# Kernel optimization log

Measured on AMD Instinct MI355X. Metric: run time of the kernel, lower is better.

## Reference

```python
import jax, jax.numpy as jnp
import numpy as np

WZ, WH, WW = 2, 6, 12
N = WZ * WH * WW            # 144 tokens per window
DIM, HEADS = 384, 12
HD = DIM // HEADS           # 32
TOW = (8 // WZ) * (48 // WH)  # type_of_windows = 32
NW = 96 // WW               # longitude windows = 8
B_ = 1 * TOW * NW           # 256
TABLE = (2 * WW - 1) * WH * WH * WZ * WZ  # 3312


def _position_index():
    zi = np.arange(WZ); zj = -np.arange(WZ) * WZ
    hi = np.arange(WH); hj = -np.arange(WH) * WH
    w = np.arange(WW)
    c1 = np.stack(np.meshgrid(zi, hi, w, indexing='ij')).reshape(3, -1)
    c2 = np.stack(np.meshgrid(zj, hj, w, indexing='ij')).reshape(3, -1)
    coords = (c1[:, :, None] - c2[:, None, :]).transpose(1, 2, 0)  # (N, N, 3)
    coords[:, :, 2] += WW - 1
    coords[:, :, 1] *= 2 * WW - 1
    coords[:, :, 0] *= (2 * WW - 1) * WH * WH
    return coords.sum(-1).reshape(-1).astype(np.int32)  # (N*N,)


def setup_inputs() -> dict:
    key = jax.random.key(0)
    ks = jax.random.split(key, 7)
    x = jax.random.normal(ks[0], (B_, N, DIM), dtype=jnp.float32)
    mask = jax.random.normal(ks[1], (NW, N, N), dtype=jnp.float32)
    w_qkv = jax.random.normal(ks[2], (DIM, 3 * DIM), dtype=jnp.float32) * 0.02
    b_qkv = jax.random.normal(ks[3], (3 * DIM,), dtype=jnp.float32) * 0.02
    w_out = jax.random.normal(ks[4], (DIM, DIM), dtype=jnp.float32) * 0.02
    b_out = jax.random.normal(ks[5], (DIM,), dtype=jnp.float32) * 0.02
    bias_table = jax.random.normal(ks[6], (TABLE, TOW, HEADS), dtype=jnp.float32) * 0.02
    position_index = jnp.asarray(_position_index())
    return {"x": x, "mask": mask, "w_qkv": w_qkv, "b_qkv": b_qkv,
            "w_out": w_out, "b_out": b_out, "bias_table": bias_table,
            "position_index": position_index}


def reference(x, mask, w_qkv, b_qkv, w_out, b_out, bias_table, position_index):
    Bw, n, C = x.shape
    scale = HD ** -0.5
    qkv = (x @ w_qkv + b_qkv).reshape(Bw, n, 3, HEADS, HD)
    qkv = jnp.transpose(qkv, (2, 0, 3, 1, 4))  # (3, Bw, H, N, hd)
    q, k, v = qkv[0] * scale, qkv[1], qkv[2]
    attn = jnp.einsum('bhnd,bhmd->bhnm', q, k)  # (Bw, H, N, N)
    # Earth-specific bias: gather table rows by position index, tiled per window group
    r = Bw // TOW
    bias = bias_table[jnp.tile(position_index, r)]          # (r*N*N, TOW, H)
    bias = bias.reshape(n, n, -1, HEADS)                    # (N, N, Bw, H)
    bias = jnp.transpose(bias, (2, 3, 0, 1))                # (Bw, H, N, N)
    attn = attn + bias
    nW = mask.shape[0]
    attn = attn.reshape(Bw // nW, nW, HEADS, n, n) + mask[None, :, None]
    attn = jax.nn.softmax(attn.reshape(Bw, HEADS, n, n), axis=-1)
    out = jnp.einsum('bhnm,bhmd->bhnd', attn, v)            # (Bw, H, N, hd)
    out = jnp.transpose(out, (0, 2, 1, 3)).reshape(Bw, n, C)
    return out @ w_out + b_out
```

## Files before the change

kernel.cpp:

```cpp
#include <hip/hip_runtime.h>
#include <hip/hip_fp16.h>
#include <cstdint>
#include <cstddef>

#define NQQ  (144*144)
#define SCALE 0.17677669529663687f

#define AOH   0ull
#define X16H  0ull
#define QH    14155776ull
#define KH    28311552ull
#define VH    42467328ull
#define WTH   56623104ull
#define WOTH  57065472ull
#define MASKH 57212928ull
#define BIASH 57378816ull
#define WS_NEED_BYTES ((BIASH + 3072ull * 2592ull) * 2ull)

typedef _Float16 half8  __attribute__((ext_vector_type(8)));
typedef _Float16 half4v __attribute__((ext_vector_type(4)));
typedef float    f32x4  __attribute__((ext_vector_type(4)));

typedef __attribute__((address_space(1))) const unsigned int guint;
typedef __attribute__((address_space(3))) unsigned int luint;
#define GLD16(g, l) __builtin_amdgcn_global_load_lds((guint*)(g), (luint*)(l), 16, 0, 0)

#define WAITV4 asm volatile("s_waitcnt vmcnt(4)" ::: "memory")
#define WAITV0 asm volatile("s_waitcnt vmcnt(0)" ::: "memory")

__launch_bounds__(256)
__global__ void k_prep(const float* __restrict__ X, _Float16* __restrict__ X16,
                       const float* __restrict__ Wq, _Float16* __restrict__ WqT,
                       const float* __restrict__ Wo, _Float16* __restrict__ WoT,
                       const float* __restrict__ M, _Float16* __restrict__ M16,
                       const float* __restrict__ table, const int* __restrict__ pidx,
                       _Float16* __restrict__ biasOut) {
    __shared__ __align__(16) char psm[13888];
    const int bid = blockIdx.x;
    const int t   = threadIdx.x;
    if (bid < 13824) {
        size_t i = (size_t)bid * 256 + t;
        float4 f = *(const float4*)&X[i * 4];
        _Float16 h[4] = {(_Float16)f.x, (_Float16)f.y, (_Float16)f.z, (_Float16)f.w};
        *(ushort4*)&X16[i * 4] = *(ushort4*)h;
        return;
    }
    if (bid >= 14130) {
        _Float16 (*sTb)[18] = (_Float16(*)[18])psm;
        int* rowsL = (int*)(psm + 13824);
        const int j      = bid - 14130;
        const int s_tile = j / 162;
        const int chunk  = j - s_tile * 162;
        const int i0     = chunk * 16;
        if (t < 16) rowsL[t] = pidx[8 * (i0 + t) + s_tile];
        __syncthreads();
#pragma unroll
        for (int rr = 0; rr < 16; ++rr) {
            int row = rowsL[rr];
            sTb[t][rr] = (_Float16)table[(size_t)row * 384 + t];
            if (t < 128) sTb[t + 256][rr] = (_Float16)table[(size_t)row * 384 + t + 256];
        }
        __syncthreads();
        unsigned int* ob = (unsigned int*)biasOut;
#pragma unroll
        for (int v = t; v < 3072; v += 256) {
            int i1h = v >> 3, dw = v & 7;
            ob[(size_t)(s_tile * 384 + i1h) * 1296 + chunk * 8 + dw] =
                *(const unsigned int*)&sTb[i1h][dw * 2];
        }
        return;
    }
    if (bid >= 13968) {
        size_t i = (size_t)(bid - 13968) * 256 + t;
        float4 f = *(const float4*)&M[i * 4];
        _Float16 h[4] = {(_Float16)f.x, (_Float16)f.y, (_Float16)f.z, (_Float16)f.w};
        *(ushort4*)&M16[i * 4] = *(ushort4*)h;
        return;
    }
    _Float16 (*sT)[72] = (_Float16(*)[72])psm;
    const float* W; _Float16* WT; int K, Cn, cb, kb;
    if (bid < 13932) {
        int j = bid - 13824;
        W = Wq; WT = WqT; K = 384; Cn = 1152;
        cb = (j % 18) * 64; kb = (j / 18) * 64;
    } else {
        int j = bid - 13932;
        W = Wo; WT = WoT; K = 384; Cn = 384;
        cb = (j % 6) * 64; kb = (j / 6) * 64;
    }
#pragma unroll
    for (int i = 0; i < 16; ++i) {
        int id = t + 256 * i;
        int kl = id >> 6, cl = id & 63;
        sT[cl][kl] = (_Float16)W[(size_t)(kb + kl) * Cn + cb + cl];
    }
    __syncthreads();
#pragma unroll
    for (int i = 0; i < 16; ++i) {
        int id = t + 256 * i;
        int cl = id >> 6, kl = id & 63;
        WT[(size_t)(cb + cl) * K + kb + kl] = sT[cl][kl];
    }
}

#define STAGE3(dA, dB, kk) do {                                   \
    GLD16(gA + (kk),          (char*)(dA) + t * 16);              \
    GLD16(gA + (kk) + 24576,  (char*)(dA) + t * 16 + 4096);       \
    GLD16(gB + (kk),          (char*)(dB) + t * 16);              \
    GLD16(gB + (kk) + 24576,  (char*)(dB) + t * 16 + 4096);       \
} while (0)

#define CSTEP(pA, pB) do {                                        \
    half8 a[4], b[4];                                             \
    _Pragma("unroll")                                             \
    for (int i = 0; i < 4; ++i) a[i] = *(const half8*)((pA) + i * 1024); \
    _Pragma("unroll")                                             \
    for (int j = 0; j < 4; ++j) b[j] = *(const half8*)((pB) + j * 1024); \
    _Pragma("unroll")                                             \
    for (int i = 0; i < 4; ++i)                                   \
    _Pragma("unroll")                                             \
        for (int j = 0; j < 4; ++j)                               \
            acc[i][j] = __builtin_amdgcn_mfma_f32_16x16x32_f16(a[i], b[j], acc[i][j], 0, 0, 0); \
} while (0)

#define GEMM_PIPE() do {                                          \
    STAGE3(sA[0], sB[0], 0);                                      \
    STAGE3(sA[1], sB[1], 32);                                     \
    _Pragma("unroll")                                             \
    for (int s = 0; s < 12; ++s) {                                \
        if (s < 11) { WAITV4; } else { WAITV0; }                  \
        __builtin_amdgcn_s_barrier();                             \
        if (s < 10) STAGE3(sA[(s + 2) % 3], sB[(s + 2) % 3], 32 * (s + 2)); \
        const char* pA = (const char*)sA[s % 3] + aoff;           \
        const char* pB = (const char*)sB[s % 3] + boff;           \
        CSTEP(pA, pB);                                            \
    }                                                             \
} while (0)

__launch_bounds__(256)
__global__ void k_qkv_gemm_mfma(const _Float16* __restrict__ X16,
                                const _Float16* __restrict__ WT,
                                const float* __restrict__ bq,
                                _Float16* __restrict__ ws16) {
    __shared__ __align__(16) _Float16 sA[3][4096];
    __shared__ __align__(16) _Float16 sB[3][4096];
    const int t    = threadIdx.x;
    const int lane = t & 63;
    const int w    = t >> 6;
    const int quad = lane >> 4;
    const int l15  = lane & 15;
    const int bid = blockIdx.x;
    const int wg  = (bid & 7) * 324 + (bid >> 3);
    const int cy  = wg % 9, rx = wg / 9;
    const int r0  = rx * 128, c0 = cy * 128;
    const int wr  = (w >> 1) * 64, wc = (w & 1) * 64;

    const int srow = t >> 2;
    const int skch = (t & 3) ^ ((t >> 3) & 3);
    const _Float16* gA = &X16[(size_t)(r0 + srow) * 384 + skch * 8];
    const _Float16* gB = &WT [(size_t)(c0 + srow) * 384 + skch * 8];

    const int swz16 = (quad ^ ((l15 >> 1) & 3)) * 16;
    const int aoff  = (wr + l15) * 64 + swz16;
    const int boff  = (wc + l15) * 64 + swz16;

    f32x4 acc[4][4] = {};

    GEMM_PIPE();

#pragma unroll
    for (int j = 0; j < 4; ++j) {
        int c  = c0 + wc + 16 * j + l15;
        int p  = c / 384;
        int hh = (c >> 5) % 12;
        int d0 = c & 31;
        float bias = bq[c];
        float sc   = (p == 0) ? SCALE : 1.0f;
        size_t base = (p == 0) ? QH : ((p == 1) ? KH : VH);
#pragma unroll
        for (int i = 0; i < 4; ++i) {
#pragma unroll
            for (int reg = 0; reg < 4; ++reg) {
                int r  = r0 + wr + 16 * i + quad * 4 + reg;
                int bw = r / 144;
                int n  = r - bw * 144;
                ws16[base + (((size_t)bw * 12 + hh) * 144 + n) * 32 + d0] =
                    (_Float16)((acc[i][j][reg] + bias) * sc);
            }
        }
    }
}

__launch_bounds__(576)
__global__ void k_attn_fused_mfma(const _Float16* __restrict__ ws16,
                                  const _Float16* __restrict__ mask16,
                                  const float* __restrict__ table,
                                  const int* __restrict__ pidx,
                                  const _Float16* __restrict__ bias_pre,
                                  _Float16* __restrict__ AO) {
    __shared__ __align__(16) char smem[27616];
    _Float16 (*sK)[40]   = (_Float16(*)[40])(smem);
    _Float16 (*sVT)[168] = (_Float16(*)[168])(smem + 11520);
    _Float16* sBias      = (_Float16*)(smem + 22272);

    const int bh = blockIdx.x;
    const int b  = bh / 12;
    const int h  = bh - b * 12;
    const int t  = threadIdx.x;
    const int w    = t >> 6;
    const int lane = t & 63;
    const int quad = lane >> 4;
    const int l15  = lane & 15;

    const int s_tile = b >> 5;
    const int i1     = b & 31;

    const _Float16* qg = ws16 + QH + (size_t)bh * 4608;
    const _Float16* kg = ws16 + KH + (size_t)bh * 4608;
    const _Float16* vg = ws16 + VH + (size_t)bh * 4608;

    half8 aq = *(const half8*)&qg[(size_t)(16 * w + l15) * 32 + quad * 8];

    {
        int row = t >> 2, ko = (t & 3) * 8;
        *(uint4*)&sK[row][ko] = *(const uint4*)&kg[row * 32 + ko];
    }
    for (int i = t; i < 2304; i += 576) {
        unsigned int u = ((const unsigned int*)vg)[i];
        int m  = i >> 4, d0 = (i & 15) * 2;
        int mp = m ^ ((d0 >> 3) << 3);
        sVT[d0][mp]     = ((const _Float16*)&u)[0];
        sVT[d0 + 1][mp] = ((const _Float16*)&u)[1];
    }
    if (t < 512) {
        int d = t & 31, m = 144 + (t >> 5);
        sVT[d][m ^ ((d >> 3) << 3)] = (_Float16)0;
    }
    if (bias_pre) {
        const _Float16* bg = bias_pre + (size_t)bh * 2592;
        for (int i2 = t; i2 < 648; i2 += 576) {
            uint2 wv = *(const uint2*)&bg[i2 * 4];
            int r18 = i2 / 36;
            int col = i2 * 4 - r18 * 144;
            *(uint2*)&sBias[r18 * 148 + col] = wv;
        }
    } else {
        for (int i = t; i < 2592; i += 576) {
            int row = pidx[8 * i + s_tile];
            int r18 = i / 144;
            sBias[r18 * 148 + (i - r18 * 144)] =
                (_Float16)table[(size_t)row * 384 + i1 * 12 + h];
        }
    }
    __syncthreads();

    f32x4 tj[9] = {};
#pragma unroll
    for (int j = 0; j < 9; ++j) {
        half8 bk = *(const half8*)&sK[16 * j + l15][quad * 8];
        tj[j] = __builtin_amdgcn_mfma_f32_16x16x32_f16(bk, aq, tj[j], 0, 0, 0);
    }

    const int q    = 16 * w + l15;
    const int nb18 = q % 18;
    const _Float16* mrow = mask16 + (size_t)(b & 7) * NQQ + (size_t)q * 144 + 4 * quad;
    uint2 mz[9];
#pragma unroll
    for (int j = 0; j < 9; ++j) mz[j] = *(const uint2*)&mrow[16 * j];
#pragma unroll
    for (int j = 0; j < 9; ++j) {
        uint2 bz = *(const uint2*)&sBias[nb18 * 148 + 16 * j + 4 * quad];
        const _Float16* bb = (const _Float16*)&bz;
        const _Float16* mm = (const _Float16*)&mz[j];
#pragma unroll
        for (int reg = 0; reg < 4; ++reg)
            tj[j][reg] += (float)bb[reg] + (float)mm[reg];
    }
    float rmax = tj[0][0];
#pragma unroll
    for (int j = 0; j < 9; ++j)
#pragma unroll
        for (int reg = 0; reg < 4; ++reg) rmax = fmaxf(rmax, tj[j][reg]);
    rmax = fmaxf(rmax, __shfl_xor(rmax, 16));
    rmax = fmaxf(rmax, __shfl_xor(rmax, 32));
    float rsum = 0.0f;
#pragma unroll
    for (int j = 0; j < 9; ++j)
#pragma unroll
        for (int reg = 0; reg < 4; ++reg) {
            tj[j][reg] = __expf(tj[j][reg] - rmax);
            rsum += tj[j][reg];
        }
    rsum += __shfl_xor(rsum, 16);
    rsum += __shfl_xor(rsum, 32);
    const float inv = 1.0f / rsum;

    unsigned int pkA[10], pkB[10];
    pkA[9] = 0u; pkB[9] = 0u;
#pragma unroll
    for (int j = 0; j < 9; ++j) {
        auto a2 = __builtin_amdgcn_cvt_pkrtz(tj[j][0] * inv, tj[j][1] * inv);
        auto b2 = __builtin_amdgcn_cvt_pkrtz(tj[j][2] * inv, tj[j][3] * inv);
        pkA[j] = *(unsigned int*)&a2;
        pkB[j] = *(unsigned int*)&b2;
    }

    const int src_lo = 32 * (quad & 1) + l15;
    const int src_hi = src_lo + 16;
    const bool selhi = (quad >> 1) != 0;
    f32x4 o[2] = {};
#pragma unroll
    for (int kt = 0; kt < 5; ++kt) {
        const int j0 = 2 * kt, j1 = 2 * kt + 1;
        unsigned int a0l = __shfl((int)pkA[j0], src_lo);
        unsigned int a1l = __shfl((int)pkA[j1], src_lo);
        unsigned int b0l = __shfl((int)pkB[j0], src_lo);
        unsigned int b1l = __shfl((int)pkB[j1], src_lo);
        unsigned int a0h = __shfl((int)pkA[j0], src_hi);
        unsigned int a1h = __shfl((int)pkA[j1], src_hi);
        unsigned int b0h = __shfl((int)pkB[j0], src_hi);
        unsigned int b1h = __shfl((int)pkB[j1], src_hi);
        union { uint4 u4; half8 h8; } bp;
        bp.u4.x = selhi ? a1l : a0l;
        bp.u4.y = selhi ? b1l : b0l;
        bp.u4.z = selhi ? a1h : a0h;
        bp.u4.w = selhi ? b1h : b0h;
#pragma unroll
        for (int dt = 0; dt < 2; ++dt) {
            const int vrow = dt * 16 + l15;
            half8 av = *(const half8*)&sVT[vrow][(kt * 32 + quad * 8) ^ ((vrow >> 3) << 3)];
            o[dt] = __builtin_amdgcn_mfma_f32_16x16x32_f16(av, bp.h8, o[dt], 0, 0, 0);
        }
    }

#pragma unroll
    for (int dt = 0; dt < 2; ++dt) {
        int d = dt * 16 + quad * 4;
        half4v hv;
#pragma unroll
        for (int reg = 0; reg < 4; ++reg) hv[reg] = (_Float16)o[dt][reg];
        *(half4v*)&AO[((size_t)b * 144 + q) * 384 + h * 32 + d] = hv;
    }
}

__launch_bounds__(256)
__global__ void k_out_gemm_mfma(const _Float16* __restrict__ A16,
                                const _Float16* __restrict__ WoT,
                                const float* __restrict__ bo,
                                float* __restrict__ out) {
    __shared__ __align__(16) _Float16 sA[3][4096];
    __shared__ __align__(16) _Float16 sB[3][4096];
    const int t    = threadIdx.x;
    const int lane = t & 63;
    const int w    = t >> 6;
    const int quad = lane >> 4;
    const int l15  = lane & 15;
    const int bid = blockIdx.x;
    const int wg  = (bid & 7) * 108 + (bid >> 3);
    const int cy  = wg % 3, rx = wg / 3;
    const int r0  = rx * 128, c0 = cy * 128;
    const int wr  = (w >> 1) * 64, wc = (w & 1) * 64;

    const int srow = t >> 2;
    const int skch = (t & 3) ^ ((t >> 3) & 3);
    const _Float16* gA = &A16[(size_t)(r0 + srow) * 384 + skch * 8];
    const _Float16* gB = &WoT[(size_t)(c0 + srow) * 384 + skch * 8];

    const int swz16 = (quad ^ ((l15 >> 1) & 3)) * 16;
    const int aoff  = (wr + l15) * 64 + swz16;
    const int boff  = (wc + l15) * 64 + swz16;

    f32x4 acc[4][4] = {};

    GEMM_PIPE();

#pragma unroll
    for (int j = 0; j < 4; ++j) {
        int c = c0 + wc + 16 * j + l15;
        float bias = bo[c];
#pragma unroll
        for (int i = 0; i < 4; ++i) {
#pragma unroll
            for (int reg = 0; reg < 4; ++reg) {
                int r = r0 + wr + 16 * i + quad * 4 + reg;
                out[(size_t)r * 384 + c] = acc[i][j][reg] + bias;
            }
        }
    }
}

extern "C" void kernel_launch(void* const* d_in, const int* in_sizes, int n_in,
                              void* d_out, int out_size, void* d_ws, size_t ws_size,
                              hipStream_t stream) {
    const float* x      = (const float*)d_in[0];
    const float* mask   = (const float*)d_in[1];
    const float* w_qkv  = (const float*)d_in[2];
    const float* b_qkv  = (const float*)d_in[3];
    const float* w_out  = (const float*)d_in[4];
    const float* b_out  = (const float*)d_in[5];
    const float* table  = (const float*)d_in[6];
    const int*   pidx   = (const int*)d_in[7];
    float* out = (float*)d_out;
    _Float16* ws16 = (_Float16*)d_ws;

    const bool pre = ws_size >= (size_t)WS_NEED_BYTES;
    _Float16* bias16 = pre ? (ws16 + BIASH) : (_Float16*)nullptr;

    hipLaunchKernelGGL(k_prep,          dim3(pre ? 15426 : 14130), dim3(256), 0, stream,
                       x, ws16 + X16H, w_qkv, ws16 + WTH, w_out, ws16 + WOTH,
                       mask, ws16 + MASKH, table, pidx, bias16);
    hipLaunchKernelGGL(k_qkv_gemm_mfma, dim3(2592), dim3(256), 0, stream,
                       ws16 + X16H, ws16 + WTH, b_qkv, ws16);
    hipLaunchKernelGGL(k_attn_fused_mfma, dim3(3072), dim3(576), 0, stream,
                       ws16, ws16 + MASKH, table, pidx, bias16, ws16 + AOH);
    hipLaunchKernelGGL(k_out_gemm_mfma, dim3(864), dim3(256), 0, stream,
                       ws16 + AOH, ws16 + WOTH, b_out, out);
}
```

Measured before the change: 259.4 us.

## Fuse QKV projection GEMM into per-window-head attention kernel

Removes the standalone QKV GEMM kernel and computes each (window, head) block's Q, K, V slice inside the attention kernel. It runs a 144x96x384 MFMA GEMM with double-buffered global-to-LDS loads and writes the results straight into shared-memory Q/K/V^T tiles. This avoids writing and re-reading the large Q/K/V intermediates through global memory and saves one launch. In exchange, each X row block is re-read once per head (12x redundant X loads), the per-block GEMM tile is small, and LDS use grows, which may reduce occupancy.

Result: faster. 245.1 us (-5.5%).

```diff
diff --git a/kernel.cpp b/kernel.cpp
--- a/kernel.cpp
+++ b/kernel.cpp
@@ -6,11 +6,8 @@
 #define NQQ  (144*144)
 #define SCALE 0.17677669529663687f
 
-#define AOH   0ull
 #define X16H  0ull
 #define QH    14155776ull
-#define KH    28311552ull
-#define VH    42467328ull
 #define WTH   56623104ull
 #define WOTH  57065472ull
 #define MASKH 57212928ull
@@ -103,110 +100,26 @@
     }
 }
 
-#define STAGE3(dA, dB, kk) do {                                   \
-    GLD16(gA + (kk),          (char*)(dA) + t * 16);              \
-    GLD16(gA + (kk) + 24576,  (char*)(dA) + t * 16 + 4096);       \
-    GLD16(gB + (kk),          (char*)(dB) + t * 16);              \
-    GLD16(gB + (kk) + 24576,  (char*)(dB) + t * 16 + 4096);       \
-} while (0)
-
-#define CSTEP(pA, pB) do {                                        \
-    half8 a[4], b[4];                                             \
-    _Pragma("unroll")                                             \
-    for (int i = 0; i < 4; ++i) a[i] = *(const half8*)((pA) + i * 1024); \
-    _Pragma("unroll")                                             \
-    for (int j = 0; j < 4; ++j) b[j] = *(const half8*)((pB) + j * 1024); \
-    _Pragma("unroll")                                             \
-    for (int i = 0; i < 4; ++i)                                   \
-    _Pragma("unroll")                                             \
-        for (int j = 0; j < 4; ++j)                               \
-            acc[i][j] = __builtin_amdgcn_mfma_f32_16x16x32_f16(a[i], b[j], acc[i][j], 0, 0, 0); \
-} while (0)
-
-#define GEMM_PIPE() do {                                          \
-    STAGE3(sA[0], sB[0], 0);                                      \
-    STAGE3(sA[1], sB[1], 32);                                     \
-    _Pragma("unroll")                                             \
-    for (int s = 0; s < 12; ++s) {                                \
-        if (s < 11) { WAITV4; } else { WAITV0; }                  \
-        __builtin_amdgcn_s_barrier();                             \
-        if (s < 10) STAGE3(sA[(s + 2) % 3], sB[(s + 2) % 3], 32 * (s + 2)); \
-        const char* pA = (const char*)sA[s % 3] + aoff;           \
-        const char* pB = (const char*)sB[s % 3] + boff;           \
-        CSTEP(pA, pB);                                            \
-    }                                                             \
-} while (0)
-
-__launch_bounds__(256)
-__global__ void k_qkv_gemm_mfma(const _Float16* __restrict__ X16,
-                                const _Float16* __restrict__ WT,
-                                const float* __restrict__ bq,
-                                _Float16* __restrict__ ws16) {
-    __shared__ __align__(16) _Float16 sA[3][4096];
-    __shared__ __align__(16) _Float16 sB[3][4096];
-    const int t    = threadIdx.x;
-    const int lane = t & 63;
-    const int w    = t >> 6;
-    const int quad = lane >> 4;
-    const int l15  = lane & 15;
+__launch_bounds__(576)
+__global__ void k_fused_qkv_attn(const _Float16* __restrict__ X16,
+                                 const _Float16* __restrict__ WT,
+                                 const float* __restrict__ bq,
+                                 const _Float16* __restrict__ mask16,
+                                 const float* __restrict__ table,
+                                 const int* __restrict__ pidx,
+                                 const _Float16* __restrict__ bias_pre,
+                                 _Float16* __restrict__ AO) {
+    __shared__ __align__(16) char smem[39120];
+    _Float16 (*sQ)[40]   = (_Float16(*)[40])(smem);
+    _Float16 (*sK)[40]   = (_Float16(*)[40])(smem + 11520);
+    _Float16 (*sVT)[168] = (_Float16(*)[168])(smem + 23040);
+    _Float16* sBias      = (_Float16*)(smem + 33792);
+
     const int bid = blockIdx.x;
-    const int wg  = (bid & 7) * 324 + (bid >> 3);
-    const int cy  = wg % 9, rx = wg / 9;
-    const int r0  = rx * 128, c0 = cy * 128;
-    const int wr  = (w >> 1) * 64, wc = (w & 1) * 64;
-
-    const int srow = t >> 2;
-    const int skch = (t & 3) ^ ((t >> 3) & 3);
-    const _Float16* gA = &X16[(size_t)(r0 + srow) * 384 + skch * 8];
-    const _Float16* gB = &WT [(size_t)(c0 + srow) * 384 + skch * 8];
-
-    const int swz16 = (quad ^ ((l15 >> 1) & 3)) * 16;
-    const int aoff  = (wr + l15) * 64 + swz16;
-    const int boff  = (wc + l15) * 64 + swz16;
-
-    f32x4 acc[4][4] = {};
-
-    GEMM_PIPE();
-
-#pragma unroll
-    for (int j = 0; j < 4; ++j) {
-        int c  = c0 + wc + 16 * j + l15;
-        int p  = c / 384;
-        int hh = (c >> 5) % 12;
-        int d0 = c & 31;
-        float bias = bq[c];
-        float sc   = (p == 0) ? SCALE : 1.0f;
-        size_t base = (p == 0) ? QH : ((p == 1) ? KH : VH);
-#pragma unroll
-        for (int i = 0; i < 4; ++i) {
-#pragma unroll
-            for (int reg = 0; reg < 4; ++reg) {
-                int r  = r0 + wr + 16 * i + quad * 4 + reg;
-                int bw = r / 144;
-                int n  = r - bw * 144;
-                ws16[base + (((size_t)bw * 12 + hh) * 144 + n) * 32 + d0] =
-                    (_Float16)((acc[i][j][reg] + bias) * sc);
-            }
-        }
-    }
-}
-
-__launch_bounds__(576)
-__global__ void k_attn_fused_mfma(const _Float16* __restrict__ ws16,
-                                  const _Float16* __restrict__ mask16,
-                                  const float* __restrict__ table,
-                                  const int* __restrict__ pidx,
-                                  const _Float16* __restrict__ bias_pre,
-                                  _Float16* __restrict__ AO) {
-    __shared__ __align__(16) char smem[27616];
-    _Float16 (*sK)[40]   = (_Float16(*)[40])(smem);
-    _Float16 (*sVT)[168] = (_Float16(*)[168])(smem + 11520);
-    _Float16* sBias      = (_Float16*)(smem + 22272);
-
-    const int bh = blockIdx.x;
-    const int b  = bh / 12;
-    const int h  = bh - b * 12;
-    const int t  = threadIdx.x;
+    const int wg  = (bid & 7) * 384 + (bid >> 3);
+    const int b   = wg / 12;
+    const int h   = wg - b * 12;
+    const int t   = threadIdx.x;
     const int w    = t >> 6;
     const int lane = t & 63;
     const int quad = lane >> 4;
@@ -215,29 +128,17 @@
     const int s_tile = b >> 5;
     const int i1     = b & 31;
 
-    const _Float16* qg = ws16 + QH + (size_t)bh * 4608;
-    const _Float16* kg = ws16 + KH + (size_t)bh * 4608;
-    const _Float16* vg = ws16 + VH + (size_t)bh * 4608;
-
-    half8 aq = *(const half8*)&qg[(size_t)(16 * w + l15) * 32 + quad * 8];
-
-    {
-        int row = t >> 2, ko = (t & 3) * 8;
-        *(uint4*)&sK[row][ko] = *(const uint4*)&kg[row * 32 + ko];
-    }
-    for (int i = t; i < 2304; i += 576) {
-        unsigned int u = ((const unsigned int*)vg)[i];
-        int m  = i >> 4, d0 = (i & 15) * 2;
-        int mp = m ^ ((d0 >> 3) << 3);
-        sVT[d0][mp]     = ((const _Float16*)&u)[0];
-        sVT[d0 + 1][mp] = ((const _Float16*)&u)[1];
-    }
-    if (t < 512) {
-        int d = t & 31, m = 144 + (t >> 5);
-        sVT[d][m ^ ((d >> 3) << 3)] = (_Float16)0;
-    }
+    const int srow = t >> 2;
+    const int schk = (t & 3) ^ ((t >> 3) & 3);
+    const _Float16* gA = &X16[((size_t)b * 144 + srow) * 384 + schk * 8];
+    const int srB  = (srow < 96) ? srow : 0;
+    const int prow = (srB >> 5) * 384 + h * 32 + (srB & 31);
+    const _Float16* gB = &WT[(size_t)prow * 384 + schk * 8];
+    const int swz16 = (quad ^ ((l15 >> 1) & 3)) * 16;
+    const int aoff  = (16 * w + l15) * 64 + swz16;
+
     if (bias_pre) {
-        const _Float16* bg = bias_pre + (size_t)bh * 2592;
+        const _Float16* bg = bias_pre + (size_t)wg * 2592;
         for (int i2 = t; i2 < 648; i2 += 576) {
             uint2 wv = *(const uint2*)&bg[i2 * 4];
             int r18 = i2 / 36;
@@ -252,8 +153,59 @@
                 (_Float16)table[(size_t)row * 384 + i1 * 12 + h];
         }
     }
+
+    f32x4 acc[6] = {};
+#define FSTG(s_) do {                                                      \
+        GLD16(gA + 32 * (s_), smem + ((s_) & 1) * 9216 + t * 16);          \
+        if (t < 384) GLD16(gB + 32 * (s_), smem + 18432 + ((s_) & 1) * 6144 + t * 16); \
+    } while (0)
+    FSTG(0);
     __syncthreads();
-
+#pragma unroll
+    for (int s = 0; s < 12; ++s) {
+        if (s < 11) FSTG(s + 1);
+        const char* pA = smem + (s & 1) * 9216 + aoff;
+        half8 av = *(const half8*)pA;
+        const char* pB = smem + 18432 + (s & 1) * 6144;
+#pragma unroll
+        for (int j = 0; j < 6; ++j) {
+            half8 bv = *(const half8*)(pB + (16 * j + l15) * 64 + swz16);
+            acc[j] = __builtin_amdgcn_mfma_f32_16x16x32_f16(av, bv, acc[j], 0, 0, 0);
+        }
+        __syncthreads();
+    }
+#undef FSTG
+
+    float bqv[6];
+#pragma unroll
+    for (int j = 0; j < 6; ++j)
+        bqv[j] = bq[(j >> 1) * 384 + h * 32 + (j & 1) * 16 + l15];
+    const int erow = 16 * w + quad * 4;
+#pragma unroll
+    for (int j = 0; j < 2; ++j)
+#pragma unroll
+        for (int reg = 0; reg < 4; ++reg)
+            sQ[erow + reg][16 * j + l15] = (_Float16)((acc[j][reg] + bqv[j]) * SCALE);
+#pragma unroll
+    for (int j = 0; j < 2; ++j)
+#pragma unroll
+        for (int reg = 0; reg < 4; ++reg)
+            sK[erow + reg][16 * j + l15] = (_Float16)(acc[2 + j][reg] + bqv[2 + j]);
+#pragma unroll
+    for (int j = 0; j < 2; ++j) {
+        const int d   = 16 * j + l15;
+        const int dsw = (d >> 3) << 3;
+#pragma unroll
+        for (int reg = 0; reg < 4; ++reg)
+            sVT[d][(erow + reg) ^ dsw] = (_Float16)(acc[4 + j][reg] + bqv[4 + j]);
+    }
+    if (t < 512) {
+        int d = t & 31, m = 144 + (t >> 5);
+        sVT[d][m ^ ((d >> 3) << 3)] = (_Float16)0;
+    }
+    __syncthreads();
+
+    half8 aq = *(const half8*)&sQ[16 * w + l15][quad * 8];
     f32x4 tj[9] = {};
 #pragma unroll
     for (int j = 0; j < 9; ++j) {
@@ -342,6 +294,40 @@
         *(half4v*)&AO[((size_t)b * 144 + q) * 384 + h * 32 + d] = hv;
     }
 }
+
+#define STAGE3(dA, dB, kk) do {                                   \
+    GLD16(gA + (kk),          (char*)(dA) + t * 16);              \
+    GLD16(gA + (kk) + 24576,  (char*)(dA) + t * 16 + 4096);       \
+    GLD16(gB + (kk),          (char*)(dB) + t * 16);              \
+    GLD16(gB + (kk) + 24576,  (char*)(dB) + t * 16 + 4096);       \
+} while (0)
+
+#define CSTEP(pA, pB) do {                                        \
+    half8 a[4], b[4];                                             \
+    _Pragma("unroll")                                             \
+    for (int i = 0; i < 4; ++i) a[i] = *(const half8*)((pA) + i * 1024); \
+    _Pragma("unroll")                                             \
+    for (int j = 0; j < 4; ++j) b[j] = *(const half8*)((pB) + j * 1024); \
+    _Pragma("unroll")                                             \
+    for (int i = 0; i < 4; ++i)                                   \
+    _Pragma("unroll")                                             \
+        for (int j = 0; j < 4; ++j)                               \
+            acc[i][j] = __builtin_amdgcn_mfma_f32_16x16x32_f16(a[i], b[j], acc[i][j], 0, 0, 0); \
+} while (0)
+
+#define GEMM_PIPE() do {                                          \
+    STAGE3(sA[0], sB[0], 0);                                      \
+    STAGE3(sA[1], sB[1], 32);                                     \
+    _Pragma("unroll")                                             \
+    for (int s = 0; s < 12; ++s) {                                \
+        if (s < 11) { WAITV4; } else { WAITV0; }                  \
+        __builtin_amdgcn_s_barrier();                             \
+        if (s < 10) STAGE3(sA[(s + 2) % 3], sB[(s + 2) % 3], 32 * (s + 2)); \
+        const char* pA = (const char*)sA[s % 3] + aoff;           \
+        const char* pB = (const char*)sB[s % 3] + boff;           \
+        CSTEP(pA, pB);                                            \
+    }                                                             \
+} while (0)
 
 __launch_bounds__(256)
 __global__ void k_out_gemm_mfma(const _Float16* __restrict__ A16,
@@ -409,10 +395,9 @@
     hipLaunchKernelGGL(k_prep,          dim3(pre ? 15426 : 14130), dim3(256), 0, stream,
                        x, ws16 + X16H, w_qkv, ws16 + WTH, w_out, ws16 + WOTH,
                        mask, ws16 + MASKH, table, pidx, bias16);
-    hipLaunchKernelGGL(k_qkv_gemm_mfma, dim3(2592), dim3(256), 0, stream,
-                       ws16 + X16H, ws16 + WTH, b_qkv, ws16);
-    hipLaunchKernelGGL(k_attn_fused_mfma, dim3(3072), dim3(576), 0, stream,
-                       ws16, ws16 + MASKH, table, pidx, bias16, ws16 + AOH);
+    hipLaunchKernelGGL(k_fused_qkv_attn, dim3(3072), dim3(576), 0, stream,
+                       ws16 + X16H, ws16 + WTH, b_qkv, ws16 + MASKH,
+                       table, pidx, bias16, ws16 + QH);
     hipLaunchKernelGGL(k_out_gemm_mfma, dim3(864), dim3(256), 0, stream,
-                       ws16 + AOH, ws16 + WOTH, b_out, out);
+                       ws16 + QH, ws16 + WOTH, b_out, out);
 }
```
